# Kernel tuning notes

Hardware: AMD Instinct MI355X
Metric: run time of the kernel (lower is better)

Reference implementation:

```python
import jax, jax.numpy as jnp
import numpy as np

N = 50000
E = 800000
IN_DIM, HID_DIM, EMB_DIM = 128, 256, 128


def _sage_conv(x, src, dst, Wp, bp, Wl, bl, Wr):
    # PyG SAGEConv(project=True, aggr='max'):
    #   x_proj = relu(x @ Wp + bp)            # projection before message passing
    #   aggr   = scatter_max(x_proj[src] -> dst)  (empty segments -> 0)
    #   out    = aggr @ Wl + bl + x @ Wr      # lin_l(aggr) + lin_r(root)
    x_proj = jax.nn.relu(x @ Wp + bp)                      # [N, in]
    msg = x_proj[src]                                      # [E, in] gather
    aggr = jax.ops.segment_max(msg, dst, num_segments=N)   # [N, in] scatter-max
    aggr = jnp.where(jnp.isneginf(aggr), 0.0, aggr)        # empty neighborhoods -> 0
    return aggr @ Wl + bl + x @ Wr


def setup_inputs() -> dict:
    key = jax.random.key(0)
    ks = jax.random.split(key, 12)
    s = 0.05
    return {
        "x": jax.random.normal(ks[0], (N, IN_DIM), dtype=jnp.float32),
        "edge_index": jax.random.randint(ks[1], (2, E), 0, N, dtype=jnp.int64),
        # layer 1 params
        "Wp1": jax.random.normal(ks[2], (IN_DIM, IN_DIM), dtype=jnp.float32) * s,
        "bp1": jnp.zeros((IN_DIM,), dtype=jnp.float32),
        "Wl1": jax.random.normal(ks[3], (IN_DIM, HID_DIM), dtype=jnp.float32) * s,
        "bl1": jnp.zeros((HID_DIM,), dtype=jnp.float32),
        "Wr1": jax.random.normal(ks[4], (IN_DIM, HID_DIM), dtype=jnp.float32) * s,
        # layer 2 params
        "Wp2": jax.random.normal(ks[5], (HID_DIM, HID_DIM), dtype=jnp.float32) * s,
        "bp2": jnp.zeros((HID_DIM,), dtype=jnp.float32),
        "Wl2": jax.random.normal(ks[6], (HID_DIM, EMB_DIM), dtype=jnp.float32) * s,
        "bl2": jnp.zeros((EMB_DIM,), dtype=jnp.float32),
        "Wr2": jax.random.normal(ks[7], (HID_DIM, EMB_DIM), dtype=jnp.float32) * s,
    }


def reference(x, edge_index, Wp1, bp1, Wl1, bl1, Wr1, Wp2, bp2, Wl2, bl2, Wr2):
    src, dst = edge_index[0], edge_index[1]
    h = jax.nn.relu(_sage_conv(x, src, dst, Wp1, bp1, Wl1, bl1, Wr1))
    h = jax.nn.relu(_sage_conv(h, src, dst, Wp2, bp2, Wl2, bl2, Wr2))
    return h
```

## Files before the change

kernel.cpp:

```cpp
#include <hip/hip_runtime.h>


typedef __attribute__((ext_vector_type(8))) short short8;
typedef __attribute__((ext_vector_type(4))) float f32x4;

#define ADJ_CAP 64
#define EPB 2048

__device__ __forceinline__ unsigned short f2bf(float f) {
    unsigned int u = __float_as_uint(f);
    u += 0x7fffu + ((u >> 16) & 1u);
    return (unsigned short)(u >> 16);
}

__device__ __forceinline__ unsigned int pkmax(unsigned int a, unsigned int b) {
    unsigned int r;
    asm("v_pk_max_u16 %0, %1, %2" : "=v"(r) : "v"(a), "v"(b));
    return r;
}

__device__ __forceinline__ short8 pack8(const float4 f0, const float4 f1) {
    union { unsigned short u[8]; short8 v; } r;
    r.u[0] = f2bf(f0.x); r.u[1] = f2bf(f0.y); r.u[2] = f2bf(f0.z); r.u[3] = f2bf(f0.w);
    r.u[4] = f2bf(f1.x); r.u[5] = f2bf(f1.y); r.u[6] = f2bf(f1.z); r.u[7] = f2bf(f1.w);
    return r.v;
}

__global__ __launch_bounds__(256) void pack_all_kernel(
    const float* __restrict__ Wp1, const float* __restrict__ Wl1,
    const float* __restrict__ Wr1, const float* __restrict__ Wp2,
    const float* __restrict__ Wl2, const float* __restrict__ Wr2,
    unsigned short* __restrict__ P0, unsigned short* __restrict__ P1,
    unsigned short* __restrict__ P3,
    unsigned short* __restrict__ P4, unsigned short* __restrict__ P5)
{
    const int idx = blockIdx.x * 256 + threadIdx.x;
    const float* W; unsigned short* P; int Nc, local, kofs = 0;
    if      (idx <  16384) { W = Wp1; P = P0; Nc = 128; local = idx; }
    else if (idx <  49152) { W = Wl1; P = P1; Nc = 256; local = idx - 16384; }
    else if (idx <  81920) { W = Wr1; P = P1; Nc = 256; local = idx - 49152; kofs = 128; }
    else if (idx < 147456) { W = Wp2; P = P3; Nc = 256; local = idx - 81920; }
    else if (idx < 180224) { W = Wl2; P = P4; Nc = 128; local = idx - 147456; }
    else if (idx < 212992) { W = Wr2; P = P5; Nc = 128; local = idx - 180224; }
    else return;
    const int k = local / Nc + kofs, c = local % Nc;
    P[((size_t)(k >> 3) * Nc + c) * 8 + (k & 7)] = f2bf(W[local]);
}

__global__ __launch_bounds__(256) void build_adj_sliced(
    const int* __restrict__ src, const int* __restrict__ dst,
    int* __restrict__ deg, unsigned short* __restrict__ padj,
    int E, int M)
{
    const int slice = blockIdx.x & 7;
    const int chunk = blockIdx.x >> 3;
    const int sliceSz = (M + 7) >> 3;
    const int lo = slice * sliceSz;
    const int hi = min(M, lo + sliceSz);
    const int base = chunk * EPB;
#pragma unroll
    for (int k = 0; k < EPB; k += 256) {
        const int e = base + k + (int)threadIdx.x;
        if (e < E) {
            const int d = dst[e];
            const int s = src[e];
            if (d >= lo && d < hi) {
                const int pos = atomicAdd(&deg[d], 1);
                if (pos < ADJ_CAP - 1)
                    padj[(size_t)d * ADJ_CAP + 1 + pos] = (unsigned short)s;
            }
        }
    }
}

__global__ __launch_bounds__(256) void projfin_kernel(
    const float* __restrict__ A,
    const unsigned short* __restrict__ W,
    const float* __restrict__ bias,
    unsigned short* __restrict__ outp,
    int M, int mbProj,
    const int* __restrict__ deg, unsigned short* __restrict__ padj)
{
    if ((int)blockIdx.x >= mbProj) {
        const int i = (blockIdx.x - mbProj) * 256 + threadIdx.x;
        if (i < M)
            padj[(size_t)i * ADJ_CAP] = (unsigned short)min(deg[i], ADJ_CAP - 1);
        return;
    }

    constexpr int K = 128, N = 128, BK = 32, LDK = BK + 8;
    __shared__ unsigned short As[64 * LDK];

    const int tid  = threadIdx.x;
    const int lane = tid & 63;
    const int wave = tid >> 6;
    const int fr   = lane & 15;
    const int g    = lane >> 4;
    const int bm   = blockIdx.x * 64;
    const int wr   = (wave >> 1) * 32;
    const int wc   = (wave & 1) * 64;

    const f32x4 zero = {0.f, 0.f, 0.f, 0.f};
    f32x4 acc[2][4];
#pragma unroll
    for (int m = 0; m < 2; ++m)
#pragma unroll
        for (int n = 0; n < 4; ++n) acc[m][n] = zero;

    for (int kt = 0; kt < K / BK; ++kt) {
        if (kt) __syncthreads();
        {
            const int r = tid >> 2, q = tid & 3;
            const int gm = min(bm + r, M - 1);
            const float4 f0 = *reinterpret_cast<const float4*>(A + (size_t)gm * K + kt * BK + q * 8);
            const float4 f1 = *reinterpret_cast<const float4*>(A + (size_t)gm * K + kt * BK + q * 8 + 4);
            *reinterpret_cast<short8*>(&As[r * LDK + q * 8]) = pack8(f0, f1);
        }
        __syncthreads();
        short8 af[2];
#pragma unroll
        for (int m = 0; m < 2; ++m)
            af[m] = *reinterpret_cast<const short8*>(&As[(wr + m * 16 + fr) * LDK + g * 8]);
#pragma unroll
        for (int n = 0; n < 4; ++n) {
            const short8 bf = *reinterpret_cast<const short8*>(
                W + ((size_t)(kt * 4 + g) * N + wc + n * 16 + fr) * 8);
#pragma unroll
            for (int m = 0; m < 2; ++m)
                acc[m][n] = __builtin_amdgcn_mfma_f32_16x16x32_bf16(af[m], bf, acc[m][n], 0, 0, 0);
        }
    }

    float bv[4];
#pragma unroll
    for (int n = 0; n < 4; ++n) bv[n] = bias[wc + n * 16 + fr];
#pragma unroll
    for (int m = 0; m < 2; ++m)
#pragma unroll
        for (int j = 0; j < 4; ++j) {
            const int row = bm + wr + m * 16 + g * 4 + j;
            if (row < M)
#pragma unroll
                for (int n = 0; n < 4; ++n)
                    outp[(size_t)row * N + wc + n * 16 + fr] =
                        f2bf(fmaxf(acc[m][n][j] + bv[n], 0.f));
        }
}

template<int D>
__global__ __launch_bounds__(256) void gather_max_bf16(
    const unsigned short* __restrict__ p, const unsigned short* __restrict__ padj,
    unsigned short* __restrict__ aggr, int n)
{
    const int node = (blockIdx.x * 256 + threadIdx.x) >> 6;
    const int lane = threadIdx.x & 63;
    if (node >= n) return;
    const int av  = (int)padj[(size_t)node * ADJ_CAP + lane];
    const int cnt = __shfl(av, 0, 64);

    if (D == 128) {
        const int q  = lane >> 4;
        const int ll = lane & 15;
        uint4 acc = make_uint4(0u, 0u, 0u, 0u);
        for (int e = 1; e <= cnt; e += 16) {
            const int r0 = __shfl(av, min(e + q,      cnt), 64);
            const int r1 = __shfl(av, min(e + 4 + q,  cnt), 64);
            const int r2 = __shfl(av, min(e + 8 + q,  cnt), 64);
            const int r3 = __shfl(av, min(e + 12 + q, cnt), 64);
            const uint4 v0 = *reinterpret_cast<const uint4*>(p + (size_t)r0 * 128 + ll * 8);
            const uint4 v1 = *reinterpret_cast<const uint4*>(p + (size_t)r1 * 128 + ll * 8);
            const uint4 v2 = *reinterpret_cast<const uint4*>(p + (size_t)r2 * 128 + ll * 8);
            const uint4 v3 = *reinterpret_cast<const uint4*>(p + (size_t)r3 * 128 + ll * 8);
            acc.x = pkmax(acc.x, pkmax(pkmax(v0.x, v1.x), pkmax(v2.x, v3.x)));
            acc.y = pkmax(acc.y, pkmax(pkmax(v0.y, v1.y), pkmax(v2.y, v3.y)));
            acc.z = pkmax(acc.z, pkmax(pkmax(v0.z, v1.z), pkmax(v2.z, v3.z)));
            acc.w = pkmax(acc.w, pkmax(pkmax(v0.w, v1.w), pkmax(v2.w, v3.w)));
        }
        acc.x = pkmax(acc.x, (unsigned int)__shfl_xor((int)acc.x, 16, 64));
        acc.y = pkmax(acc.y, (unsigned int)__shfl_xor((int)acc.y, 16, 64));
        acc.z = pkmax(acc.z, (unsigned int)__shfl_xor((int)acc.z, 16, 64));
        acc.w = pkmax(acc.w, (unsigned int)__shfl_xor((int)acc.w, 16, 64));
        acc.x = pkmax(acc.x, (unsigned int)__shfl_xor((int)acc.x, 32, 64));
        acc.y = pkmax(acc.y, (unsigned int)__shfl_xor((int)acc.y, 32, 64));
        acc.z = pkmax(acc.z, (unsigned int)__shfl_xor((int)acc.z, 32, 64));
        acc.w = pkmax(acc.w, (unsigned int)__shfl_xor((int)acc.w, 32, 64));
        if (lane < 16)
            *reinterpret_cast<uint4*>(aggr + (size_t)node * 128 + ll * 8) = acc;
    } else {
        const int h  = lane >> 5;
        const int ll = lane & 31;
        uint4 acc = make_uint4(0u, 0u, 0u, 0u);
        for (int e = 1; e <= cnt; e += 16) {
            const int r0 = __shfl(av, min(e + h,      cnt), 64);
            const int r1 = __shfl(av, min(e + 2 + h,  cnt), 64);
            const int r2 = __shfl(av, min(e + 4 + h,  cnt), 64);
            const int r3 = __shfl(av, min(e + 6 + h,  cnt), 64);
            const int r4 = __shfl(av, min(e + 8 + h,  cnt), 64);
            const int r5 = __shfl(av, min(e + 10 + h, cnt), 64);
            const int r6 = __shfl(av, min(e + 12 + h, cnt), 64);
            const int r7 = __shfl(av, min(e + 14 + h, cnt), 64);
            const uint4 v0 = *reinterpret_cast<const uint4*>(p + (size_t)r0 * 256 + ll * 8);
            const uint4 v1 = *reinterpret_cast<const uint4*>(p + (size_t)r1 * 256 + ll * 8);
            const uint4 v2 = *reinterpret_cast<const uint4*>(p + (size_t)r2 * 256 + ll * 8);
            const uint4 v3 = *reinterpret_cast<const uint4*>(p + (size_t)r3 * 256 + ll * 8);
            const uint4 v4 = *reinterpret_cast<const uint4*>(p + (size_t)r4 * 256 + ll * 8);
            const uint4 v5 = *reinterpret_cast<const uint4*>(p + (size_t)r5 * 256 + ll * 8);
            const uint4 v6 = *reinterpret_cast<const uint4*>(p + (size_t)r6 * 256 + ll * 8);
            const uint4 v7 = *reinterpret_cast<const uint4*>(p + (size_t)r7 * 256 + ll * 8);
            acc.x = pkmax(acc.x, pkmax(pkmax(pkmax(v0.x, v1.x), pkmax(v2.x, v3.x)),
                                        pkmax(pkmax(v4.x, v5.x), pkmax(v6.x, v7.x))));
            acc.y = pkmax(acc.y, pkmax(pkmax(pkmax(v0.y, v1.y), pkmax(v2.y, v3.y)),
                                        pkmax(pkmax(v4.y, v5.y), pkmax(v6.y, v7.y))));
            acc.z = pkmax(acc.z, pkmax(pkmax(pkmax(v0.z, v1.z), pkmax(v2.z, v3.z)),
                                        pkmax(pkmax(v4.z, v5.z), pkmax(v6.z, v7.z))));
            acc.w = pkmax(acc.w, pkmax(pkmax(pkmax(v0.w, v1.w), pkmax(v2.w, v3.w)),
                                        pkmax(pkmax(v4.w, v5.w), pkmax(v6.w, v7.w))));
        }
        acc.x = pkmax(acc.x, (unsigned int)__shfl_xor((int)acc.x, 32, 64));
        acc.y = pkmax(acc.y, (unsigned int)__shfl_xor((int)acc.y, 32, 64));
        acc.z = pkmax(acc.z, (unsigned int)__shfl_xor((int)acc.z, 32, 64));
        acc.w = pkmax(acc.w, (unsigned int)__shfl_xor((int)acc.w, 32, 64));
        if (lane < 32)
            *reinterpret_cast<uint4*>(aggr + (size_t)node * 256 + ll * 8) = acc;
    }
}

__global__ __launch_bounds__(256) void tail1_kernel(
    const unsigned short* __restrict__ a1,
    const float* __restrict__ x,
    const unsigned short* __restrict__ Wcat,
    const float* __restrict__ bl,
    const unsigned short* __restrict__ Wp2,
    const float* __restrict__ bp2,
    unsigned short* __restrict__ h1,
    unsigned short* __restrict__ p2,
    int M)
{
    constexpr int LDH = 264;
    __shared__ unsigned short Hs[32 * LDH];

    const int tid  = threadIdx.x;
    const int lane = tid & 63;
    const int wave = tid >> 6;
    const int fr   = lane & 15;
    const int g    = lane >> 4;
    const int bm   = blockIdx.x * 32;
    const int wc   = wave * 64;

    const f32x4 zero = {0.f, 0.f, 0.f, 0.f};
    f32x4 acc[2][4];
#pragma unroll
    for (int m = 0; m < 2; ++m)
#pragma unroll
        for (int n = 0; n < 4; ++n) acc[m][n] = zero;

#pragma unroll
    for (int c = 0; c < 4; ++c) {
        const int t = tid + c * 256;
        const int r = t >> 5, q = t & 31;
        const int gm = min(bm + r, M - 1);
        short8 v;
        if (q < 16) {
            v = *reinterpret_cast<const short8*>(a1 + (size_t)gm * 128 + q * 8);
        } else {
            const float4 f0 = *reinterpret_cast<const float4*>(x + (size_t)gm * 128 + (q - 16) * 8);
            const float4 f1 = *reinterpret_cast<const float4*>(x + (size_t)gm * 128 + (q - 16) * 8 + 4);
            v = pack8(f0, f1);
        }
        *reinterpret_cast<short8*>(&Hs[r * LDH + q * 8]) = v;
    }
    __syncthreads();
#pragma unroll
    for (int kt = 0; kt < 8; ++kt) {
        short8 af[2];
#pragma unroll
        for (int m = 0; m < 2; ++m)
            af[m] = *reinterpret_cast<const short8*>(&Hs[(m * 16 + fr) * LDH + kt * 32 + g * 8]);
#pragma unroll
        for (int n = 0; n < 4; ++n) {
            const short8 bf = *reinterpret_cast<const short8*>(
                Wcat + ((size_t)(kt * 4 + g) * 256 + wc + n * 16 + fr) * 8);
#pragma unroll
            for (int m = 0; m < 2; ++m)
                acc[m][n] = __builtin_amdgcn_mfma_f32_16x16x32_bf16(af[m], bf, acc[m][n], 0, 0, 0);
        }
    }
    __syncthreads();

    {
        float bv[4];
#pragma unroll
        for (int n = 0; n < 4; ++n) bv[n] = bl[wc + n * 16 + fr];
#pragma unroll
        for (int m = 0; m < 2; ++m)
#pragma unroll
            for (int j = 0; j < 4; ++j) {
                const int rl = m * 16 + g * 4 + j;
#pragma unroll
                for (int n = 0; n < 4; ++n) {
                    const unsigned short hb = f2bf(fmaxf(acc[m][n][j] + bv[n], 0.f));
                    Hs[rl * LDH + wc + n * 16 + fr] = hb;
                    if (bm + rl < M)
                        h1[(size_t)(bm + rl) * 256 + wc + n * 16 + fr] = hb;
                }
            }
    }
    __syncthreads();

#pragma unroll
    for (int m = 0; m < 2; ++m)
#pragma unroll
        for (int n = 0; n < 4; ++n) acc[m][n] = zero;
#pragma unroll
    for (int kt = 0; kt < 8; ++kt) {
        short8 af[2];
#pragma unroll
        for (int m = 0; m < 2; ++m)
            af[m] = *reinterpret_cast<const short8*>(&Hs[(m * 16 + fr) * LDH + kt * 32 + g * 8]);
#pragma unroll
        for (int n = 0; n < 4; ++n) {
            const short8 bf = *reinterpret_cast<const short8*>(
                Wp2 + ((size_t)(kt * 4 + g) * 256 + wc + n * 16 + fr) * 8);
#pragma unroll
            for (int m = 0; m < 2; ++m)
                acc[m][n] = __builtin_amdgcn_mfma_f32_16x16x32_bf16(af[m], bf, acc[m][n], 0, 0, 0);
        }
    }
    {
        float bv[4];
#pragma unroll
        for (int n = 0; n < 4; ++n) bv[n] = bp2[wc + n * 16 + fr];
#pragma unroll
        for (int m = 0; m < 2; ++m)
#pragma unroll
            for (int j = 0; j < 4; ++j) {
                const int row = bm + m * 16 + g * 4 + j;
                if (row < M)
#pragma unroll
                    for (int n = 0; n < 4; ++n)
                        p2[(size_t)row * 256 + wc + n * 16 + fr] =
                            f2bf(fmaxf(acc[m][n][j] + bv[n], 0.f));
            }
    }
}

__global__ __launch_bounds__(256) void tail2_kernel(
    const unsigned short* __restrict__ a2,
    const unsigned short* __restrict__ h1,
    const unsigned short* __restrict__ Wl,
    const unsigned short* __restrict__ Wr,
    const float* __restrict__ bl,
    float* __restrict__ out, int M)
{
    constexpr int LDK = 264;
    __shared__ unsigned short As[32 * LDK];

    const int tid  = threadIdx.x;
    const int lane = tid & 63;
    const int wave = tid >> 6;
    const int fr   = lane & 15;
    const int g    = lane >> 4;
    const int bm   = blockIdx.x * 32;
    const int wc   = wave * 32;

    const f32x4 zero = {0.f, 0.f, 0.f, 0.f};
    f32x4 acc[2][2];
#pragma unroll
    for (int m = 0; m < 2; ++m)
#pragma unroll
        for (int n = 0; n < 2; ++n) acc[m][n] = zero;

#pragma unroll
    for (int ph = 0; ph < 2; ++ph) {
        const unsigned short* __restrict__ P = ph ? h1 : a2;
        const unsigned short* __restrict__ W = ph ? Wr : Wl;
        if (ph) __syncthreads();
#pragma unroll
        for (int c = 0; c < 4; ++c) {
            const int t = tid + c * 256;
            const int r = t >> 5, q = t & 31;
            const int gm = min(bm + r, M - 1);
            *reinterpret_cast<short8*>(&As[r * LDK + q * 8]) =
                *reinterpret_cast<const short8*>(P + (size_t)gm * 256 + q * 8);
        }
        __syncthreads();
#pragma unroll
        for (int kt = 0; kt < 8; ++kt) {
            short8 af[2];
#pragma unroll
            for (int m = 0; m < 2; ++m)
                af[m] = *reinterpret_cast<const short8*>(&As[(m * 16 + fr) * LDK + kt * 32 + g * 8]);
#pragma unroll
            for (int n = 0; n < 2; ++n) {
                const short8 bf = *reinterpret_cast<const short8*>(
                    W + ((size_t)(kt * 4 + g) * 128 + wc + n * 16 + fr) * 8);
#pragma unroll
                for (int m = 0; m < 2; ++m)
                    acc[m][n] = __builtin_amdgcn_mfma_f32_16x16x32_bf16(af[m], bf, acc[m][n], 0, 0, 0);
            }
        }
    }

    float bv[2];
#pragma unroll
    for (int n = 0; n < 2; ++n) bv[n] = bl[wc + n * 16 + fr];
#pragma unroll
    for (int m = 0; m < 2; ++m)
#pragma unroll
        for (int j = 0; j < 4; ++j) {
            const int row = bm + m * 16 + g * 4 + j;
            if (row < M)
#pragma unroll
                for (int n = 0; n < 2; ++n)
                    out[(size_t)row * 128 + wc + n * 16 + fr] =
                        fmaxf(acc[m][n][j] + bv[n], 0.f);
        }
}

extern "C" void kernel_launch(void* const* d_in, const int* in_sizes, int n_in,
                              void* d_out, int out_size, void* d_ws, size_t ws_size,
                              hipStream_t stream)
{
    const float* x   = (const float*)d_in[0];
    const int*   ei  = (const int*)d_in[1];
    const float* Wp1 = (const float*)d_in[2];
    const float* bp1 = (const float*)d_in[3];
    const float* Wl1 = (const float*)d_in[4];
    const float* bl1 = (const float*)d_in[5];
    const float* Wr1 = (const float*)d_in[6];
    const float* Wp2 = (const float*)d_in[7];
    const float* bp2 = (const float*)d_in[8];
    const float* Wl2 = (const float*)d_in[9];
    const float* bl2 = (const float*)d_in[10];
    const float* Wr2 = (const float*)d_in[11];
    float* out = (float*)d_out;

    const int M = in_sizes[0] / 128;
    const int E = in_sizes[1] / 2;
    const int* src = ei;
    const int* dst = ei + E;

    unsigned short* ws  = (unsigned short*)d_ws;
    unsigned short* p1b = ws;
    unsigned short* a1b = p1b + (size_t)M * 128;
    unsigned short* h1b = a1b + (size_t)M * 128;
    unsigned short* p2b = h1b + (size_t)M * 256;
    unsigned short* a2b = p2b + (size_t)M * 256;
    unsigned short* wpk = a2b + (size_t)M * 256;
    unsigned short* Wp1p  = wpk;
    unsigned short* Wcat1 = Wp1p + 128 * 128;
    unsigned short* Wp2p  = Wcat1 + 256 * 256;
    unsigned short* Wl2p  = Wp2p + 256 * 256;
    unsigned short* Wr2p  = Wl2p + 256 * 128;
    unsigned short* endu  = Wr2p + 256 * 128;
    size_t off = ((size_t)(endu - ws) * 2 + 127) & ~(size_t)127;
    unsigned short* padj = (unsigned short*)((char*)d_ws + off);
    size_t off2 = (off + (size_t)M * ADJ_CAP * 2 + 127) & ~(size_t)127;
    int* deg = (int*)((char*)d_ws + off2);

    const dim3 blk(256);
    const int gb = (M + 3) / 4;
    const int mb64 = (M + 63) / 64;
    const int mb32 = (M + 31) / 32;
    const int fb = (M + 255) / 256;
    const int nChunks = (E + EPB - 1) / EPB;

    pack_all_kernel<<<(212992 + 255) / 256, blk, 0, stream>>>(
        Wp1, Wl1, Wr1, Wp2, Wl2, Wr2, Wp1p, Wcat1, Wp2p, Wl2p, Wr2p);
    hipMemsetAsync(deg, 0, (size_t)M * sizeof(int), stream);
    build_adj_sliced<<<8 * nChunks, blk, 0, stream>>>(src, dst, deg, padj, E, M);
    projfin_kernel<<<mb64 + fb, blk, 0, stream>>>(
        x, Wp1p, bp1, p1b, M, mb64, deg, padj);

    gather_max_bf16<128><<<gb, blk, 0, stream>>>(p1b, padj, a1b, M);
    tail1_kernel<<<mb32, blk, 0, stream>>>(
        a1b, x, Wcat1, bl1, Wp2p, bp2, h1b, p2b, M);

    gather_max_bf16<256><<<gb, blk, 0, stream>>>(p2b, padj, a2b, M);
    tail2_kernel<<<mb32, blk, 0, stream>>>(
        a2b, h1b, Wl2p, Wr2p, bl2, out, M);
}
```

Before: 194.0 us.

## Bucket adjacency by source range and phase gathers for cache locality

Result: slower. 220.1 us (+13.4%).

```diff
diff --git a/kernel.cpp b/kernel.cpp
--- a/kernel.cpp
+++ b/kernel.cpp
@@ -4,7 +4,7 @@
 typedef __attribute__((ext_vector_type(8))) short short8;
 typedef __attribute__((ext_vector_type(4))) float f32x4;
 
-#define ADJ_CAP 64
+#define BSLOT 15
 #define EPB 2048
 
 __device__ __forceinline__ unsigned short f2bf(float f) {
@@ -24,6 +24,11 @@
     r.u[0] = f2bf(f0.x); r.u[1] = f2bf(f0.y); r.u[2] = f2bf(f0.z); r.u[3] = f2bf(f0.w);
     r.u[4] = f2bf(f1.x); r.u[5] = f2bf(f1.y); r.u[6] = f2bf(f1.z); r.u[7] = f2bf(f1.w);
     return r.v;
+}
+
+__device__ __forceinline__ int xshort(int reg, int j) {
+    const int t = __shfl(reg, j >> 1, 64);
+    return (t >> ((j & 1) << 4)) & 0xffff;
 }
 
 __global__ __launch_bounds__(256) void pack_all_kernel(
@@ -49,14 +54,14 @@
 
 __global__ __launch_bounds__(256) void build_adj_sliced(
     const int* __restrict__ src, const int* __restrict__ dst,
-    int* __restrict__ deg, unsigned short* __restrict__ padj,
-    int E, int M)
+    int* __restrict__ deg8, unsigned short* __restrict__ padj,
+    int E, int M, int sliceSz)
 {
     const int slice = blockIdx.x & 7;
     const int chunk = blockIdx.x >> 3;
-    const int sliceSz = (M + 7) >> 3;
-    const int lo = slice * sliceSz;
-    const int hi = min(M, lo + sliceSz);
+    const int dSz = (M + 7) >> 3;
+    const int lo = slice * dSz;
+    const int hi = min(M, lo + dSz);
     const int base = chunk * EPB;
 #pragma unroll
     for (int k = 0; k < EPB; k += 256) {
@@ -65,9 +70,10 @@
             const int d = dst[e];
             const int s = src[e];
             if (d >= lo && d < hi) {
-                const int pos = atomicAdd(&deg[d], 1);
-                if (pos < ADJ_CAP - 1)
-                    padj[(size_t)d * ADJ_CAP + 1 + pos] = (unsigned short)s;
+                const int b = s / sliceSz;
+                const int pos = atomicAdd(&deg8[d * 8 + b], 1);
+                if (pos < BSLOT)
+                    padj[(size_t)d * 128 + 8 + b * BSLOT + pos] = (unsigned short)s;
             }
         }
     }
@@ -79,12 +85,14 @@
     const float* __restrict__ bias,
     unsigned short* __restrict__ outp,
     int M, int mbProj,
-    const int* __restrict__ deg, unsigned short* __restrict__ padj)
+    const int* __restrict__ deg8, unsigned short* __restrict__ padj)
 {
     if ((int)blockIdx.x >= mbProj) {
         const int i = (blockIdx.x - mbProj) * 256 + threadIdx.x;
-        if (i < M)
-            padj[(size_t)i * ADJ_CAP] = (unsigned short)min(deg[i], ADJ_CAP - 1);
+        if (i < M * 8) {
+            const int n = i >> 3, b = i & 7;
+            padj[(size_t)n * 128 + b] = (unsigned short)min(deg8[i], BSLOT);
+        }
         return;
     }
 
@@ -147,82 +155,73 @@
         }
 }
 
-template<int D>
-__global__ __launch_bounds__(256) void gather_max_bf16(
+__global__ __launch_bounds__(256, 8) void gather1_phased(
+    const unsigned short* __restrict__ p, const unsigned short* __restrict__ padj,
+    unsigned short* __restrict__ aggr, int n)
+{
+    const int lane = threadIdx.x & 63;
+    const int gw   = (blockIdx.x * 256 + threadIdx.x) >> 6;
+
+    int row[7]; unsigned int acc[7]; bool ok[7];
+#pragma unroll
+    for (int k = 0; k < 7; ++k) {
+        const int nd = gw + k * 8192;
+        ok[k] = (nd < n);
+        acc[k] = 0u;
+        row[k] = ok[k]
+            ? *reinterpret_cast<const int*>(padj + (size_t)nd * 128 + lane * 2)
+            : 0;
+    }
+
+    for (int s = 0; s < 8; ++s) {
+#pragma unroll
+        for (int k = 0; k < 7; ++k) {
+            if (!ok[k]) continue;
+            const int cnt = xshort(row[k], s);
+            const int jb  = 8 + s * BSLOT;
+            for (int e = 0; e < cnt; ++e) {
+                const int srcid = xshort(row[k], jb + e);
+                const unsigned int v = *reinterpret_cast<const unsigned int*>(
+                    p + (size_t)srcid * 128 + lane * 2);
+                acc[k] = pkmax(acc[k], v);
+            }
+        }
+    }
+
+#pragma unroll
+    for (int k = 0; k < 7; ++k)
+        if (ok[k])
+            *reinterpret_cast<unsigned int*>(
+                aggr + (size_t)(gw + k * 8192) * 128 + lane * 2) = acc[k];
+}
+
+__global__ __launch_bounds__(256) void gather2_bucket(
     const unsigned short* __restrict__ p, const unsigned short* __restrict__ padj,
     unsigned short* __restrict__ aggr, int n)
 {
     const int node = (blockIdx.x * 256 + threadIdx.x) >> 6;
     const int lane = threadIdx.x & 63;
     if (node >= n) return;
-    const int av  = (int)padj[(size_t)node * ADJ_CAP + lane];
-    const int cnt = __shfl(av, 0, 64);
-
-    if (D == 128) {
-        const int q  = lane >> 4;
-        const int ll = lane & 15;
-        uint4 acc = make_uint4(0u, 0u, 0u, 0u);
-        for (int e = 1; e <= cnt; e += 16) {
-            const int r0 = __shfl(av, min(e + q,      cnt), 64);
-            const int r1 = __shfl(av, min(e + 4 + q,  cnt), 64);
-            const int r2 = __shfl(av, min(e + 8 + q,  cnt), 64);
-            const int r3 = __shfl(av, min(e + 12 + q, cnt), 64);
-            const uint4 v0 = *reinterpret_cast<const uint4*>(p + (size_t)r0 * 128 + ll * 8);
-            const uint4 v1 = *reinterpret_cast<const uint4*>(p + (size_t)r1 * 128 + ll * 8);
-            const uint4 v2 = *reinterpret_cast<const uint4*>(p + (size_t)r2 * 128 + ll * 8);
-            const uint4 v3 = *reinterpret_cast<const uint4*>(p + (size_t)r3 * 128 + ll * 8);
+    const int row = *reinterpret_cast<const int*>(padj + (size_t)node * 128 + lane * 2);
+
+    uint2 acc = make_uint2(0u, 0u);
+    for (int s = 0; s < 8; ++s) {
+        const int cnt = xshort(row, s);
+        const int jb  = 8 + s * BSLOT;
+        for (int e = 0; e < cnt; e += 4) {
+            const int s0 = xshort(row, jb + e);
+            const int s1 = xshort(row, jb + min(e + 1, cnt - 1));
+            const int s2 = xshort(row, jb + min(e + 2, cnt - 1));
+            const int s3 = xshort(row, jb + min(e + 3, cnt - 1));
+            const uint2 v0 = *reinterpret_cast<const uint2*>(p + (size_t)s0 * 256 + lane * 4);
+            const uint2 v1 = *reinterpret_cast<const uint2*>(p + (size_t)s1 * 256 + lane * 4);
+            const uint2 v2 = *reinterpret_cast<const uint2*>(p + (size_t)s2 * 256 + lane * 4);
+            const uint2 v3 = *reinterpret_cast<const uint2*>(p + (size_t)s3 * 256 + lane * 4);
             acc.x = pkmax(acc.x, pkmax(pkmax(v0.x, v1.x), pkmax(v2.x, v3.x)));
             acc.y = pkmax(acc.y, pkmax(pkmax(v0.y, v1.y), pkmax(v2.y, v3.y)));
-            acc.z = pkmax(acc.z, pkmax(pkmax(v0.z, v1.z), pkmax(v2.z, v3.z)));
-            acc.w = pkmax(acc.w, pkmax(pkmax(v0.w, v1.w), pkmax(v2.w, v3.w)));
-        }
-        acc.x = pkmax(acc.x, (unsigned int)__shfl_xor((int)acc.x, 16, 64));
-        acc.y = pkmax(acc.y, (unsigned int)__shfl_xor((int)acc.y, 16, 64));
-        acc.z = pkmax(acc.z, (unsigned int)__shfl_xor((int)acc.z, 16, 64));
-        acc.w = pkmax(acc.w, (unsigned int)__shfl_xor((int)acc.w, 16, 64));
-        acc.x = pkmax(acc.x, (unsigned int)__shfl_xor((int)acc.x, 32, 64));
-        acc.y = pkmax(acc.y, (unsigned int)__shfl_xor((int)acc.y, 32, 64));
-        acc.z = pkmax(acc.z, (unsigned int)__shfl_xor((int)acc.z, 32, 64));
-        acc.w = pkmax(acc.w, (unsigned int)__shfl_xor((int)acc.w, 32, 64));
-        if (lane < 16)
-            *reinterpret_cast<uint4*>(aggr + (size_t)node * 128 + ll * 8) = acc;
-    } else {
-        const int h  = lane >> 5;
-        const int ll = lane & 31;
-        uint4 acc = make_uint4(0u, 0u, 0u, 0u);
-        for (int e = 1; e <= cnt; e += 16) {
-            const int r0 = __shfl(av, min(e + h,      cnt), 64);
-            const int r1 = __shfl(av, min(e + 2 + h,  cnt), 64);
-            const int r2 = __shfl(av, min(e + 4 + h,  cnt), 64);
-            const int r3 = __shfl(av, min(e + 6 + h,  cnt), 64);
-            const int r4 = __shfl(av, min(e + 8 + h,  cnt), 64);
-            const int r5 = __shfl(av, min(e + 10 + h, cnt), 64);
-            const int r6 = __shfl(av, min(e + 12 + h, cnt), 64);
-            const int r7 = __shfl(av, min(e + 14 + h, cnt), 64);
-            const uint4 v0 = *reinterpret_cast<const uint4*>(p + (size_t)r0 * 256 + ll * 8);
-            const uint4 v1 = *reinterpret_cast<const uint4*>(p + (size_t)r1 * 256 + ll * 8);
-            const uint4 v2 = *reinterpret_cast<const uint4*>(p + (size_t)r2 * 256 + ll * 8);
-            const uint4 v3 = *reinterpret_cast<const uint4*>(p + (size_t)r3 * 256 + ll * 8);
-            const uint4 v4 = *reinterpret_cast<const uint4*>(p + (size_t)r4 * 256 + ll * 8);
-            const uint4 v5 = *reinterpret_cast<const uint4*>(p + (size_t)r5 * 256 + ll * 8);
-            const uint4 v6 = *reinterpret_cast<const uint4*>(p + (size_t)r6 * 256 + ll * 8);
-            const uint4 v7 = *reinterpret_cast<const uint4*>(p + (size_t)r7 * 256 + ll * 8);
-            acc.x = pkmax(acc.x, pkmax(pkmax(pkmax(v0.x, v1.x), pkmax(v2.x, v3.x)),
-                                        pkmax(pkmax(v4.x, v5.x), pkmax(v6.x, v7.x))));
-            acc.y = pkmax(acc.y, pkmax(pkmax(pkmax(v0.y, v1.y), pkmax(v2.y, v3.y)),
-                                        pkmax(pkmax(v4.y, v5.y), pkmax(v6.y, v7.y))));
-            acc.z = pkmax(acc.z, pkmax(pkmax(pkmax(v0.z, v1.z), pkmax(v2.z, v3.z)),
-                                        pkmax(pkmax(v4.z, v5.z), pkmax(v6.z, v7.z))));
-            acc.w = pkmax(acc.w, pkmax(pkmax(pkmax(v0.w, v1.w), pkmax(v2.w, v3.w)),
-                                        pkmax(pkmax(v4.w, v5.w), pkmax(v6.w, v7.w))));
-        }
-        acc.x = pkmax(acc.x, (unsigned int)__shfl_xor((int)acc.x, 32, 64));
-        acc.y = pkmax(acc.y, (unsigned int)__shfl_xor((int)acc.y, 32, 64));
-        acc.z = pkmax(acc.z, (unsigned int)__shfl_xor((int)acc.z, 32, 64));
-        acc.w = pkmax(acc.w, (unsigned int)__shfl_xor((int)acc.w, 32, 64));
-        if (lane < 32)
-            *reinterpret_cast<uint4*>(aggr + (size_t)node * 256 + ll * 8) = acc;
-    }
+        }
+    }
+    *reinterpret_cast<uint2*>(aggr + (size_t)node * 256 + lane * 4) = acc;
 }
 
 __global__ __launch_bounds__(256) void tail1_kernel(
@@ -439,6 +438,7 @@
     const int E = in_sizes[1] / 2;
     const int* src = ei;
     const int* dst = ei + E;
+    const int sliceSz = (M + 7) / 8;
 
     unsigned short* ws  = (unsigned short*)d_ws;
     unsigned short* p1b = ws;
@@ -453,30 +453,31 @@
     unsigned short* Wl2p  = Wp2p + 256 * 256;
     unsigned short* Wr2p  = Wl2p + 256 * 128;
     unsigned short* endu  = Wr2p + 256 * 128;
-    size_t off = ((size_t)(endu - ws) * 2 + 127) & ~(size_t)127;
+    size_t off = ((size_t)(endu - ws) * 2 + 255) & ~(size_t)255;
     unsigned short* padj = (unsigned short*)((char*)d_ws + off);
-    size_t off2 = (off + (size_t)M * ADJ_CAP * 2 + 127) & ~(size_t)127;
-    int* deg = (int*)((char*)d_ws + off2);
+    size_t off2 = (off + (size_t)M * 128 * 2 + 127) & ~(size_t)127;
+    int* deg8 = (int*)((char*)d_ws + off2);
 
     const dim3 blk(256);
     const int gb = (M + 3) / 4;
     const int mb64 = (M + 63) / 64;
     const int mb32 = (M + 31) / 32;
-    const int fb = (M + 255) / 256;
+    const int fb = (M * 8 + 255) / 256;
     const int nChunks = (E + EPB - 1) / EPB;
 
     pack_all_kernel<<<(212992 + 255) / 256, blk, 0, stream>>>(
         Wp1, Wl1, Wr1, Wp2, Wl2, Wr2, Wp1p, Wcat1, Wp2p, Wl2p, Wr2p);
-    hipMemsetAsync(deg, 0, (size_t)M * sizeof(int), stream);
-    build_adj_sliced<<<8 * nChunks, blk, 0, stream>>>(src, dst, deg, padj, E, M);
+    hipMemsetAsync(deg8, 0, (size_t)M * 8 * sizeof(int), stream);
+    build_adj_sliced<<<8 * nChunks, blk, 0, stream>>>(
+        src, dst, deg8, padj, E, M, sliceSz);
     projfin_kernel<<<mb64 + fb, blk, 0, stream>>>(
-        x, Wp1p, bp1, p1b, M, mb64, deg, padj);
-
-    gather_max_bf16<128><<<gb, blk, 0, stream>>>(p1b, padj, a1b, M);
+        x, Wp1p, bp1, p1b, M, mb64, deg8, padj);
+
+    gather1_phased<<<2048, blk, 0, stream>>>(p1b, padj, a1b, M);
     tail1_kernel<<<mb32, blk, 0, stream>>>(
         a1b, x, Wcat1, bl1, Wp2p, bp2, h1b, p2b, M);
 
-    gather_max_bf16<256><<<gb, blk, 0, stream>>>(p2b, padj, a2b, M);
+    gather2_bucket<<<gb, blk, 0, stream>>>(p2b, padj, a2b, M);
     tail2_kernel<<<mb32, blk, 0, stream>>>(
         a2b, h1b, Wl2p, Wr2p, bl2, out, M);
 }
```
